# Kernel tuning notes

Measured on AMD Instinct MI355X. Metric: run time of the kernel, lower is better.

## Reference

```python
import jax, jax.numpy as jnp
import numpy as np

EPS = 1e-5
DN = ('NCDHW', 'OIDHW', 'NCDHW')

def conv3d(x, w, b):
    y = jax.lax.conv_general_dilated(x, w, (1, 1, 1), 'SAME', dimension_numbers=DN)
    return y + b[None, :, None, None, None]

def batchnorm(x, gamma, beta):
    # training-mode BatchNorm3d: biased batch stats over (N, D, H, W) per channel
    mean = jnp.mean(x, axis=(0, 2, 3, 4), keepdims=True)
    var = jnp.mean((x - mean) ** 2, axis=(0, 2, 3, 4), keepdims=True)
    xhat = (x - mean) * jax.lax.rsqrt(var + EPS)
    return gamma[None, :, None, None, None] * xhat + beta[None, :, None, None, None]

def setup_inputs() -> dict:
    key = jax.random.key(0)
    ks = jax.random.split(key, 8)
    C, N = 32, 4  # channel, fuzzynum
    B, D, H, W = 4, 64, 64, 64
    x = jax.random.normal(ks[0], (B, C, D, H, W), dtype=jnp.float32)
    fan1 = C * 27
    conv1_w = jax.random.uniform(ks[1], (1, C, 3, 3, 3), jnp.float32, -1, 1) / np.sqrt(fan1)
    conv1_b = jnp.zeros((1,), jnp.float32)
    fan2 = 1 * 27
    conv2_w = jax.random.uniform(ks[2], (C, 1, 3, 3, 3), jnp.float32, -1, 1) / np.sqrt(fan2)
    conv2_b = jnp.zeros((C,), jnp.float32)
    mu = jax.random.normal(ks[3], (C, N), dtype=jnp.float32)
    sigma = jax.random.normal(ks[4], (C, N), dtype=jnp.float32)
    bn1_g = jnp.ones((1,), jnp.float32)
    bn1_b = jnp.zeros((1,), jnp.float32)
    bn2_g = jnp.ones((C,), jnp.float32)
    bn2_b = jnp.zeros((C,), jnp.float32)
    return {"x": x, "conv1_w": conv1_w, "conv1_b": conv1_b, "conv2_w": conv2_w,
            "conv2_b": conv2_b, "mu": mu, "sigma": sigma,
            "bn1_g": bn1_g, "bn1_b": bn1_b, "bn2_g": bn2_g, "bn2_b": bn2_b}

def reference(x, conv1_w, conv1_b, conv2_w, conv2_b, mu, sigma, bn1_g, bn1_b, bn2_g, bn2_b):
    x1 = conv3d(x, conv1_w, conv1_b)                      # [B,1,D,H,W]
    # fuzzy Gaussian membership: only channel 0 of mu/sigma is used (x1 has 1 channel)
    m = mu[0]                                             # [n]
    s = sigma[0]                                          # [n]
    z = (x1[..., None] - m) / s                           # [B,1,D,H,W,n]
    fuzz = jnp.exp(-jnp.sum(z * z, axis=-1))              # [B,1,D,H,W]
    y = batchnorm(fuzz, bn1_g, bn1_b)
    y = conv3d(y, conv2_w, conv2_b)                       # [B,C,D,H,W]
    return batchnorm(y, bn2_g, bn2_b)
```

## Files before the change

kernel.cpp:

```cpp
#include <hip/hip_runtime.h>

constexpr int Cc = 32;
constexpr int SP = 64 * 64 * 64;
constexpr int TS = 4 * SP;

constexpr int PW  = 68;
constexpr int PZR = 66 * PW;
constexpr int PSP = 66 * PZR;
constexpr int PTOT = 4 * PSP;

constexpr int WOFF  = 68 + 64 * 64;
constexpr int ACC_N = WOFF + 864;

__global__ __launch_bounds__(256) void k_conv1_fuzzy(
    const float* __restrict__ x, const float* __restrict__ w1,
    const float* __restrict__ b1, const float* __restrict__ mu,
    const float* __restrict__ sg, float* __restrict__ fuzz,
    float* __restrict__ acc)
{
    const int tid = threadIdx.x;
    const int t = blockIdx.x * 256 + tid;
    const int wq = t & 15;        const int w0 = wq << 2;
    const int z  = (t >> 4) & 63;
    const int y  = (t >> 10) & 63;
    const int b  = t >> 16;
    const int lane = tid & 63;

    float S1 = 0.f, S2 = 0.f, S3 = 0.f;
#pragma unroll
    for (int n = 0; n < 4; n++) {
        float m = mu[n], s = sg[n];
        float iv = 1.0f / (s * s);
        S1 += iv; S2 += m * iv; S3 += m * m * iv;
    }

    const float b1v = b1[0];
    float a0 = b1v, a1 = b1v, a2 = b1v, a3 = b1v;

    const float* xb = x + (size_t)b * Cc * SP;

    bool pv[9]; int ofs[9];
#pragma unroll
    for (int rz = 0; rz < 3; rz++) {
        const int zz = z - 1 + rz;
        const int zzc = min(max(zz, 0), 63);
        const bool okz = (unsigned)zz < 64u;
#pragma unroll
        for (int dy = 0; dy < 3; dy++) {
            const int yy = y - 1 + dy;
            const int yyc = min(max(yy, 0), 63);
            pv[rz * 3 + dy]  = okz && ((unsigned)yy < 64u);
            ofs[rz * 3 + dy] = (zzc << 12) + (yyc << 6) + w0;
        }
    }

    auto LOADCH = [&](int c, float4 (&M)[9]) {
        const float* xc = xb + (size_t)c * SP;
#pragma unroll
        for (int i = 0; i < 9; i++)
            M[i] = *(const float4*)(xc + ofs[i]);
    };

    auto COMPUTECH = [&](int c, float4 (&M)[9]) {
#pragma unroll
        for (int i = 0; i < 9; i++) {
            M[i].x = pv[i] ? M[i].x : 0.f;
            M[i].y = pv[i] ? M[i].y : 0.f;
            M[i].z = pv[i] ? M[i].z : 0.f;
            M[i].w = pv[i] ? M[i].w : 0.f;
        }
        const float* wc = w1 + c * 27;
        float Wv[27];
#pragma unroll
        for (int k = 0; k < 27; k++) Wv[k] = wc[k];
#pragma unroll
        for (int i = 0; i < 9; i++) {
            const float4 m = M[i];
            const float lv = __shfl(m.w, (lane + 63) & 63, 64);
            const float rv = __shfl(m.x, (lane + 1) & 63, 64);
            const float v0 = (wq > 0)  ? lv : 0.f;
            const float v5 = (wq < 15) ? rv : 0.f;
            const float W0 = Wv[i * 3], W1 = Wv[i * 3 + 1], W2 = Wv[i * 3 + 2];
            a0 = fmaf(v0,  W0, fmaf(m.x, W1, fmaf(m.y, W2, a0)));
            a1 = fmaf(m.x, W0, fmaf(m.y, W1, fmaf(m.z, W2, a1)));
            a2 = fmaf(m.y, W0, fmaf(m.z, W1, fmaf(m.w, W2, a2)));
            a3 = fmaf(m.z, W0, fmaf(m.w, W1, fmaf(v5,  W2, a3)));
        }
    };

    float4 Ma[9], Mb[9];
    LOADCH(0, Ma);
    for (int c = 0; c < Cc; c += 2) {
        LOADCH(c + 1, Mb);
        COMPUTECH(c, Ma);
        if (c + 2 < Cc) LOADCH(c + 2, Ma);
        COMPUTECH(c + 1, Mb);
    }

    float fsum = 0.f, fsq = 0.f;
    float xv[4] = { a0, a1, a2, a3 };
    float* fp = fuzz + (size_t)b * PSP + (size_t)(z + 1) * PZR
              + (y + 1) * PW + (w0 + 1);
#pragma unroll
    for (int ow = 0; ow < 4; ow++) {
        float x1 = xv[ow];
        float tt = x1 * x1 * S1 - 2.0f * x1 * S2 + S3;
        float fz = __expf(-tt);
        fp[ow] = fz; fsum += fz; fsq += fz * fz;
    }
#pragma unroll
    for (int m = 1; m < 64; m <<= 1) {
        fsum += __shfl_xor(fsum, m, 64);
        fsq  += __shfl_xor(fsq,  m, 64);
    }
    __shared__ float red[8];
    const int wid = tid >> 6;
    if ((tid & 63) == 0) { red[wid * 2] = fsum; red[wid * 2 + 1] = fsq; }
    __syncthreads();
    if (tid == 0) {
        atomicAdd(&acc[0], red[0] + red[2] + red[4] + red[6]);
        atomicAdd(&acc[1], red[1] + red[3] + red[5] + red[7]);
    }
}

__global__ void k_fin1(const float* __restrict__ g, const float* __restrict__ be,
                       const float* __restrict__ w2, float* __restrict__ acc)
{
    const int tid = threadIdx.x;
    if (tid == 0) {
        float mean = acc[0] * (1.0f / TS);
        float var  = acc[1] * (1.0f / TS) - mean * mean;
        float a = g[0] * rsqrtf(var + 1e-5f);
        acc[2] = a;
        acc[3] = be[0] - mean * a;
    }
    if (tid < 864) {
        const int c   = tid / 27;
        const int cls = tid - c * 27;
        const int zc  = cls / 9;
        const int r   = cls - zc * 9;
        const int yc  = r / 3;
        const int xc  = r - yc * 3;
        float s = 0.f;
#pragma unroll
        for (int dz = 0; dz < 3; dz++) {
            if ((zc == 0 && dz == 0) || (zc == 2 && dz == 2)) continue;
#pragma unroll
            for (int dy = 0; dy < 3; dy++) {
                if ((yc == 0 && dy == 0) || (yc == 2 && dy == 2)) continue;
#pragma unroll
                for (int dx = 0; dx < 3; dx++) {
                    if ((xc == 0 && dx == 0) || (xc == 2 && dx == 2)) continue;
                    s += w2[c * 27 + (dz * 3 + dy) * 3 + dx];
                }
            }
        }
        acc[WOFF + tid] = s;
    }
}

template <bool WRITE>
__global__ __launch_bounds__(256) void k_conv2(
    const float* __restrict__ fuzz, const float* __restrict__ w2,
    const float* __restrict__ b2, const float* __restrict__ g2,
    const float* __restrict__ be2, float* __restrict__ acc,
    float* __restrict__ out)
{
    const int tid = threadIdx.x;
    const int lane = tid & 63;
    const int wid = __builtin_amdgcn_readfirstlane(tid >> 6);
    const int bi = blockIdx.x;
    const int w = lane;
    const int y = bi & 63;
    const int z0 = ((bi >> 6) & 15) << 2;
    const int b = bi >> 10;
    const float a = acc[2], sh = acc[3];
    const float* fb = fuzz + (size_t)b * PSP;
    const int c0 = wid * 8;

    float scv[8], shv[8];
    if (WRITE) {
#pragma unroll
        for (int ci = 0; ci < 8; ci++) {
            const int c = c0 + ci;
            float s = acc[68 + c * 64 + lane];
            float q = acc[68 + (32 + c) * 64 + lane];
#pragma unroll
            for (int mm = 1; mm < 64; mm <<= 1) {
                s += __shfl_xor(s, mm, 64);
                q += __shfl_xor(q, mm, 64);
            }
            const float mean = s * (1.0f / TS);
            const float var  = q * (1.0f / TS) - mean * mean;
            const float sc = g2[c] * rsqrtf(var + 1e-5f);
            scv[ci] = sc;
            shv[ci] = be2[c] - mean * sc;
        }
    }

    float Fl[6][3], Fm[6][3], Fr[6][3];
#pragma unroll
    for (int rz = 0; rz < 6; rz++) {
#pragma unroll
        for (int dy = 0; dy < 3; dy++) {
            const float* rp = fb + (size_t)(z0 + rz) * PZR + (y + dy) * PW + w;
            Fl[rz][dy] = rp[0];
            Fm[rz][dy] = rp[1];
            Fr[rz][dy] = rp[2];
        }
    }

    const int yc  = (y == 0) ? 0 : ((y == 63) ? 2 : 1);
    const int zc0 = (z0 == 0) ? 0 : 1;
    const int zc3 = (z0 + 3 == 63) ? 2 : 1;
    const bool lo = (lane == 0), hi = (lane == 63);

    float* ob = out + (size_t)b * Cc * SP + (z0 << 12) + (y << 6) + w;
    const int slot = bi & 63;

#pragma unroll
    for (int ci = 0; ci < 8; ci++) {
        const int c = c0 + ci;
        const float* wc = w2 + c * 27;
        float Wv[27];
#pragma unroll
        for (int k = 0; k < 27; k++) Wv[k] = wc[k];
        float o0 = 0.f, o1 = 0.f, o2 = 0.f, o3 = 0.f;
#pragma unroll
        for (int rz = 0; rz < 6; rz++) {
#pragma unroll
            for (int dy = 0; dy < 3; dy++) {
                const float l = Fl[rz][dy], m = Fm[rz][dy], r = Fr[rz][dy];
#pragma unroll
                for (int oz = 0; oz < 4; oz++) {
                    const int dz = rz - oz;
                    if (dz < 0 || dz > 2) continue;
                    const float W0 = Wv[(dz*3+dy)*3], W1 = Wv[(dz*3+dy)*3+1], W2 = Wv[(dz*3+dy)*3+2];
                    if      (oz == 0) o0 = fmaf(l, W0, fmaf(m, W1, fmaf(r, W2, o0)));
                    else if (oz == 1) o1 = fmaf(l, W0, fmaf(m, W1, fmaf(r, W2, o1)));
                    else if (oz == 2) o2 = fmaf(l, W0, fmaf(m, W1, fmaf(r, W2, o2)));
                    else              o3 = fmaf(l, W0, fmaf(m, W1, fmaf(r, W2, o3)));
                }
            }
        }
        const float bb = b2[c];
        const float* tb = acc + WOFF + c * 27 + yc * 3;
        const float* t0 = tb + zc0 * 9;
        const float* t1 = tb + 9;
        const float* t3 = tb + zc3 * 9;
        const float w0s = lo ? t0[0] : (hi ? t0[2] : t0[1]);
        const float w1s = lo ? t1[0] : (hi ? t1[2] : t1[1]);
        const float w3s = lo ? t3[0] : (hi ? t3[2] : t3[1]);
        const float off0 = fmaf(sh, w0s, bb);
        const float off1 = fmaf(sh, w1s, bb);
        const float off3 = fmaf(sh, w3s, bb);
        const float v0 = fmaf(o0, a, off0);
        const float v1 = fmaf(o1, a, off1);
        const float v2 = fmaf(o2, a, off1);
        const float v3 = fmaf(o3, a, off3);

        if (WRITE) {
            const float sc = scv[ci], s2 = shv[ci];
            ob[(size_t)c * SP]         = fmaf(v0, sc, s2);
            ob[(size_t)c * SP + 4096]  = fmaf(v1, sc, s2);
            ob[(size_t)c * SP + 8192]  = fmaf(v2, sc, s2);
            ob[(size_t)c * SP + 12288] = fmaf(v3, sc, s2);
        } else {
            float ps = (v0 + v1) + (v2 + v3);
            float pq = fmaf(v0, v0, fmaf(v1, v1, fmaf(v2, v2, v3 * v3)));
#pragma unroll
            for (int mm = 1; mm < 64; mm <<= 1) {
                ps += __shfl_xor(ps, mm, 64);
                pq += __shfl_xor(pq, mm, 64);
            }
            if (lane == 0) {
                atomicAdd(&acc[68 + c * 64 + slot], ps);
                atomicAdd(&acc[68 + (32 + c) * 64 + slot], pq);
            }
        }
    }
}

extern "C" void kernel_launch(void* const* d_in, const int* in_sizes, int n_in,
                              void* d_out, int out_size, void* d_ws, size_t ws_size,
                              hipStream_t stream)
{
    const float* x   = (const float*)d_in[0];
    const float* w1  = (const float*)d_in[1];
    const float* b1  = (const float*)d_in[2];
    const float* w2  = (const float*)d_in[3];
    const float* b2  = (const float*)d_in[4];
    const float* mu  = (const float*)d_in[5];
    const float* sg  = (const float*)d_in[6];
    const float* g1  = (const float*)d_in[7];
    const float* be1 = (const float*)d_in[8];
    const float* g2  = (const float*)d_in[9];
    const float* be2 = (const float*)d_in[10];

    float* out  = (float*)d_out;
    float* fuzz = (float*)d_ws;
    float* acc  = fuzz + PTOT;

    hipMemsetAsync(fuzz, 0, (size_t)(PTOT + ACC_N) * sizeof(float), stream);
    k_conv1_fuzzy<<<1024, 256, 0, stream>>>(x, w1, b1, mu, sg, fuzz, acc);
    k_fin1<<<1, 864, 0, stream>>>(g1, be1, w2, acc);
    k_conv2<false><<<4096, 256, 0, stream>>>(fuzz, w2, b2, g2, be2, acc, out);
    k_conv2<true><<<4096, 256, 0, stream>>>(fuzz, w2, b2, g2, be2, acc, out);
}
```

Before: 370.2 us.

## Fuse conv2 stats with output write and add separate BN2 apply pass

Replaces the two-pass conv2 (stats pass then recompute-and-write pass) with a single pass that writes unnormalized output while accumulating channel statistics, followed by an elementwise kernel that normalizes the output in place. Also replaces cross-lane shuffles in conv1 with direct neighbor scalar loads. This removes the conv2 recomputation but adds a full extra read and write of the large output tensor.

New measurement: 469.1 us. +26.7%, slower.

```diff
diff --git a/kernel.cpp b/kernel.cpp
--- a/kernel.cpp
+++ b/kernel.cpp
@@ -24,7 +24,6 @@
     const int z  = (t >> 4) & 63;
     const int y  = (t >> 10) & 63;
     const int b  = t >> 16;
-    const int lane = tid & 63;
 
     float S1 = 0.f, S2 = 0.f, S3 = 0.f;
 #pragma unroll
@@ -39,7 +38,9 @@
 
     const float* xb = x + (size_t)b * Cc * SP;
 
-    bool pv[9]; int ofs[9];
+    bool pv[9], pl[9], pr[9]; int ofs[9];
+    const int dL = (wq > 0)  ? 1 : 0;
+    const int dR = (wq < 15) ? 4 : 3;
 #pragma unroll
     for (int rz = 0; rz < 3; rz++) {
         const int zz = z - 1 + rz;
@@ -49,26 +50,25 @@
         for (int dy = 0; dy < 3; dy++) {
             const int yy = y - 1 + dy;
             const int yyc = min(max(yy, 0), 63);
-            pv[rz * 3 + dy]  = okz && ((unsigned)yy < 64u);
+            const bool ok = okz && ((unsigned)yy < 64u);
+            pv[rz * 3 + dy]  = ok;
+            pl[rz * 3 + dy]  = ok && (wq > 0);
+            pr[rz * 3 + dy]  = ok && (wq < 15);
             ofs[rz * 3 + dy] = (zzc << 12) + (yyc << 6) + w0;
         }
     }
 
-    auto LOADCH = [&](int c, float4 (&M)[9]) {
+    auto LOADCH = [&](int c, float4 (&M)[9], float (&L)[9], float (&R)[9]) {
         const float* xc = xb + (size_t)c * SP;
 #pragma unroll
-        for (int i = 0; i < 9; i++)
+        for (int i = 0; i < 9; i++) {
             M[i] = *(const float4*)(xc + ofs[i]);
+            L[i] = xc[ofs[i] - dL];
+            R[i] = xc[ofs[i] + dR];
+        }
     };
 
-    auto COMPUTECH = [&](int c, float4 (&M)[9]) {
-#pragma unroll
-        for (int i = 0; i < 9; i++) {
-            M[i].x = pv[i] ? M[i].x : 0.f;
-            M[i].y = pv[i] ? M[i].y : 0.f;
-            M[i].z = pv[i] ? M[i].z : 0.f;
-            M[i].w = pv[i] ? M[i].w : 0.f;
-        }
+    auto COMPUTECH = [&](int c, float4 (&M)[9], float (&L)[9], float (&R)[9]) {
         const float* wc = w1 + c * 27;
         float Wv[27];
 #pragma unroll
@@ -76,25 +76,28 @@
 #pragma unroll
         for (int i = 0; i < 9; i++) {
             const float4 m = M[i];
-            const float lv = __shfl(m.w, (lane + 63) & 63, 64);
-            const float rv = __shfl(m.x, (lane + 1) & 63, 64);
-            const float v0 = (wq > 0)  ? lv : 0.f;
-            const float v5 = (wq < 15) ? rv : 0.f;
+            const float v1 = pv[i] ? m.x : 0.f;
+            const float v2 = pv[i] ? m.y : 0.f;
+            const float v3 = pv[i] ? m.z : 0.f;
+            const float v4 = pv[i] ? m.w : 0.f;
+            const float v0 = pl[i] ? L[i] : 0.f;
+            const float v5 = pr[i] ? R[i] : 0.f;
             const float W0 = Wv[i * 3], W1 = Wv[i * 3 + 1], W2 = Wv[i * 3 + 2];
-            a0 = fmaf(v0,  W0, fmaf(m.x, W1, fmaf(m.y, W2, a0)));
-            a1 = fmaf(m.x, W0, fmaf(m.y, W1, fmaf(m.z, W2, a1)));
-            a2 = fmaf(m.y, W0, fmaf(m.z, W1, fmaf(m.w, W2, a2)));
-            a3 = fmaf(m.z, W0, fmaf(m.w, W1, fmaf(v5,  W2, a3)));
+            a0 = fmaf(v0, W0, fmaf(v1, W1, fmaf(v2, W2, a0)));
+            a1 = fmaf(v1, W0, fmaf(v2, W1, fmaf(v3, W2, a1)));
+            a2 = fmaf(v2, W0, fmaf(v3, W1, fmaf(v4, W2, a2)));
+            a3 = fmaf(v3, W0, fmaf(v4, W1, fmaf(v5, W2, a3)));
         }
     };
 
     float4 Ma[9], Mb[9];
-    LOADCH(0, Ma);
+    float La[9], Ra[9], Lb[9], Rb[9];
+    LOADCH(0, Ma, La, Ra);
     for (int c = 0; c < Cc; c += 2) {
-        LOADCH(c + 1, Mb);
-        COMPUTECH(c, Ma);
-        if (c + 2 < Cc) LOADCH(c + 2, Ma);
-        COMPUTECH(c + 1, Mb);
+        LOADCH(c + 1, Mb, Lb, Rb);
+        COMPUTECH(c, Ma, La, Ra);
+        if (c + 2 < Cc) LOADCH(c + 2, Ma, La, Ra);
+        COMPUTECH(c + 1, Mb, Lb, Rb);
     }
 
     float fsum = 0.f, fsq = 0.f;
@@ -159,11 +162,9 @@
     }
 }
 
-template <bool WRITE>
-__global__ __launch_bounds__(256) void k_conv2(
+__global__ __launch_bounds__(256) void k_conv2_fused(
     const float* __restrict__ fuzz, const float* __restrict__ w2,
-    const float* __restrict__ b2, const float* __restrict__ g2,
-    const float* __restrict__ be2, float* __restrict__ acc,
+    const float* __restrict__ b2, float* __restrict__ acc,
     float* __restrict__ out)
 {
     const int tid = threadIdx.x;
@@ -177,26 +178,6 @@
     const float a = acc[2], sh = acc[3];
     const float* fb = fuzz + (size_t)b * PSP;
     const int c0 = wid * 8;
-
-    float scv[8], shv[8];
-    if (WRITE) {
-#pragma unroll
-        for (int ci = 0; ci < 8; ci++) {
-            const int c = c0 + ci;
-            float s = acc[68 + c * 64 + lane];
-            float q = acc[68 + (32 + c) * 64 + lane];
-#pragma unroll
-            for (int mm = 1; mm < 64; mm <<= 1) {
-                s += __shfl_xor(s, mm, 64);
-                q += __shfl_xor(q, mm, 64);
-            }
-            const float mean = s * (1.0f / TS);
-            const float var  = q * (1.0f / TS) - mean * mean;
-            const float sc = g2[c] * rsqrtf(var + 1e-5f);
-            scv[ci] = sc;
-            shv[ci] = be2[c] - mean * sc;
-        }
-    }
 
     float Fl[6][3], Fm[6][3], Fr[6][3];
 #pragma unroll
@@ -259,26 +240,57 @@
         const float v2 = fmaf(o2, a, off1);
         const float v3 = fmaf(o3, a, off3);
 
-        if (WRITE) {
-            const float sc = scv[ci], s2 = shv[ci];
-            ob[(size_t)c * SP]         = fmaf(v0, sc, s2);
-            ob[(size_t)c * SP + 4096]  = fmaf(v1, sc, s2);
-            ob[(size_t)c * SP + 8192]  = fmaf(v2, sc, s2);
-            ob[(size_t)c * SP + 12288] = fmaf(v3, sc, s2);
-        } else {
-            float ps = (v0 + v1) + (v2 + v3);
-            float pq = fmaf(v0, v0, fmaf(v1, v1, fmaf(v2, v2, v3 * v3)));
-#pragma unroll
-            for (int mm = 1; mm < 64; mm <<= 1) {
-                ps += __shfl_xor(ps, mm, 64);
-                pq += __shfl_xor(pq, mm, 64);
-            }
-            if (lane == 0) {
-                atomicAdd(&acc[68 + c * 64 + slot], ps);
-                atomicAdd(&acc[68 + (32 + c) * 64 + slot], pq);
-            }
-        }
-    }
+        ob[(size_t)c * SP]         = v0;
+        ob[(size_t)c * SP + 4096]  = v1;
+        ob[(size_t)c * SP + 8192]  = v2;
+        ob[(size_t)c * SP + 12288] = v3;
+
+        float ps = (v0 + v1) + (v2 + v3);
+        float pq = fmaf(v0, v0, fmaf(v1, v1, fmaf(v2, v2, v3 * v3)));
+#pragma unroll
+        for (int mm = 1; mm < 64; mm <<= 1) {
+            ps += __shfl_xor(ps, mm, 64);
+            pq += __shfl_xor(pq, mm, 64);
+        }
+        if (lane == 0) {
+            atomicAdd(&acc[68 + c * 64 + slot], ps);
+            atomicAdd(&acc[68 + (32 + c) * 64 + slot], pq);
+        }
+    }
+}
+
+__global__ __launch_bounds__(256) void k_bn2_apply(
+    const float* __restrict__ g2, const float* __restrict__ be2,
+    const float* __restrict__ acc, float* __restrict__ out)
+{
+    const int tid = threadIdx.x;
+    const int t = blockIdx.x * 256 + tid;
+    const int c = (t >> 16) & 31;
+    __shared__ float bc[2];
+    if (tid < 64) {
+        float s = acc[68 + c * 64 + tid];
+        float q = acc[68 + (32 + c) * 64 + tid];
+#pragma unroll
+        for (int mm = 1; mm < 64; mm <<= 1) {
+            s += __shfl_xor(s, mm, 64);
+            q += __shfl_xor(q, mm, 64);
+        }
+        if (tid == 0) {
+            const float mean = s * (1.0f / TS);
+            const float var  = q * (1.0f / TS) - mean * mean;
+            const float sc = g2[c] * rsqrtf(var + 1e-5f);
+            bc[0] = sc;
+            bc[1] = be2[c] - mean * sc;
+        }
+    }
+    __syncthreads();
+    const float sc = bc[0], shf = bc[1];
+    float4 v = ((const float4*)out)[t];
+    v.x = fmaf(v.x, sc, shf);
+    v.y = fmaf(v.y, sc, shf);
+    v.z = fmaf(v.z, sc, shf);
+    v.w = fmaf(v.w, sc, shf);
+    ((float4*)out)[t] = v;
 }
 
 extern "C" void kernel_launch(void* const* d_in, const int* in_sizes, int n_in,
@@ -304,6 +316,6 @@
     hipMemsetAsync(fuzz, 0, (size_t)(PTOT + ACC_N) * sizeof(float), stream);
     k_conv1_fuzzy<<<1024, 256, 0, stream>>>(x, w1, b1, mu, sg, fuzz, acc);
     k_fin1<<<1, 864, 0, stream>>>(g1, be1, w2, acc);
-    k_conv2<false><<<4096, 256, 0, stream>>>(fuzz, w2, b2, g2, be2, acc, out);
-    k_conv2<true><<<4096, 256, 0, stream>>>(fuzz, w2, b2, g2, be2, acc, out);
-}
+    k_conv2_fused<<<4096, 256, 0, stream>>>(fuzz, w2, b2, acc, out);
+    k_bn2_apply<<<32768, 256, 0, stream>>>(g2, be2, acc, out);
+}
```
